# Optimization experiments

Measured on AMD Instinct MI355X. Metric: run time of the kernel, lower is better.

Reference implementation:

```python
import jax, jax.numpy as jnp
import numpy as np

N_NODES = 100_000
N_EDGES = 3_200_000
F_IN, HID, OUT = 64, 64, 6


def setup_inputs() -> dict:
    key = jax.random.key(0)
    k1, k2, k3, k4 = jax.random.split(key, 4)
    x = jax.random.normal(k1, (N_NODES, F_IN), dtype=jnp.float32)
    edge_index = jax.random.randint(k2, (2, N_EDGES), 0, N_NODES, dtype=jnp.int32)
    W1 = jax.random.normal(k3, (F_IN, HID), dtype=jnp.float32) * (1.0 / np.sqrt(F_IN))
    b1 = jnp.zeros((HID,), dtype=jnp.float32)
    W2 = jax.random.normal(k4, (HID, OUT), dtype=jnp.float32) * (1.0 / np.sqrt(HID))
    b2 = jnp.zeros((OUT,), dtype=jnp.float32)
    return {"x": x, "edge_index": edge_index, "W1": W1, "b1": b1, "W2": W2, "b2": b2}


def _gcn_conv(x, row, col, norm, W, b):
    # x: [N, F_in], row/col/norm: [E'], W: [F_in, F_out]
    n = x.shape[0]
    h = x @ W                                   # [N, F_out]
    msg = h[row] * norm[:, None]                # gather + scale, [E', F_out]
    out = jax.ops.segment_sum(msg, col, num_segments=n)  # scatter-add to targets
    return out + b


def reference(x, edge_index, W1, b1, W2, b2):
    n = x.shape[0]
    # add self-loops (PyG GCNConv default)
    loops = jnp.arange(n, dtype=edge_index.dtype)
    row = jnp.concatenate([edge_index[0], loops])  # source
    col = jnp.concatenate([edge_index[1], loops])  # target
    # symmetric normalization: deg computed at target incl. self-loops
    deg = jax.ops.segment_sum(jnp.ones_like(col, dtype=x.dtype), col, num_segments=n)
    dinv = jnp.where(deg > 0, jax.lax.rsqrt(deg), 0.0)
    norm = dinv[row] * dinv[col]                # [E']

    h = jax.nn.relu(_gcn_conv(x, row, col, norm, W1, b1))
    out = _gcn_conv(h, row, col, norm, W2, b2)
    return jnp.mean(out, axis=0)                # [OUT]
```

## Files before the change

### kernel.cpp

```cpp
#include <hip/hip_runtime.h>

#define N_NODES 100000
#define N_EDGES 3200000
#define NOUT 6

#define NPB 256
#define NBUK ((N_NODES + NPB - 1) / NPB)
#define CAP 12288
#define PCHUNK 4096
#define PNB ((N_EDGES + PCHUNK - 1) / PCHUNK)
#define SORT_CAP 10240
#define AGB (N_NODES / 32)
#define NPART (2 * AGB)

typedef __attribute__((ext_vector_type(2))) float v2f;

__global__ __launch_bounds__(512) void k_initcur(int* __restrict__ gcursor) {
    int t = threadIdx.x;
    if (t < NBUK) gcursor[t] = t * CAP;
}

__global__ __launch_bounds__(512) void k_partition(const int* __restrict__ row,
                                                   const int* __restrict__ col,
                                                   int* __restrict__ gcursor,
                                                   int* __restrict__ bedge) {
    __shared__ int hist[512];
    __shared__ int lstart[512];
    __shared__ int lcur[512];
    __shared__ int gbase[512];
    __shared__ int sscan[512];
    __shared__ int stage[PCHUNK];
    __shared__ unsigned short stageb[PCHUNK];

    const int t = threadIdx.x;
    const int c0 = blockIdx.x * PCHUNK;
    int cnt = N_EDGES - c0; if (cnt > PCHUNK) cnt = PCHUNK;

    hist[t] = 0; lcur[t] = 0;
    __syncthreads();

    int myp[8]; int myb[8];
#pragma unroll
    for (int i = 0; i < 8; ++i) {
        int p = i * 512 + t;
        myb[i] = -1;
        if (p < cnt) {
            int e = c0 + p;
            int c = col[e], r = row[e];
            int b = c >> 8;
            myp[i] = ((c & 255) << 17) | r;
            myb[i] = b;
            atomicAdd(&hist[b], 1);
        }
    }
    __syncthreads();

    int hv = hist[t];
    sscan[t] = hv;
    __syncthreads();
    for (int off = 1; off < 512; off <<= 1) {
        int u = (t >= off) ? sscan[t - off] : 0;
        __syncthreads();
        sscan[t] += u;
        __syncthreads();
    }
    lstart[t] = sscan[t] - hv;
    if (t < NBUK && hv > 0) gbase[t] = atomicAdd(&gcursor[t], hv);
    __syncthreads();

#pragma unroll
    for (int i = 0; i < 8; ++i) {
        if (myb[i] >= 0) {
            int pos = lstart[myb[i]] + atomicAdd(&lcur[myb[i]], 1);
            stage[pos] = myp[i];
            stageb[pos] = (unsigned short)myb[i];
        }
    }
    __syncthreads();

    for (int p = t; p < cnt; p += 512) {
        int b = stageb[p];
        int dst = gbase[b] + p - lstart[b];
        if (dst < (b + 1) * CAP) bedge[dst] = stage[p];
    }
}

__global__ __launch_bounds__(512) void k_bucket_sort(const int* __restrict__ gcursor,
                                                     const int* __restrict__ bedge,
                                                     float* __restrict__ dinv,
                                                     int* __restrict__ node_off,
                                                     int* __restrict__ sorted_row) {
    __shared__ int cnt[NPB];
    __shared__ int lstart[NPB];
    __shared__ int lcur[NPB];
    __shared__ int sc[NPB];
    __shared__ int stage[SORT_CAP];

    const int t = threadIdx.x;
    const int b = blockIdx.x;
    const int s = b * CAP;
    int m = gcursor[b] - s; if (m > CAP) m = CAP;
    const bool fits = (m <= SORT_CAP);

    if (t < NPB) { cnt[t] = 0; lcur[t] = 0; }
    __syncthreads();

    if (fits) {
        for (int j = t; j < m; j += 512) {
            int p = bedge[s + j];
            stage[j] = p;
            atomicAdd(&cnt[p >> 17], 1);
        }
    } else {
        for (int j = t; j < m; j += 512) atomicAdd(&cnt[bedge[s + j] >> 17], 1);
    }
    __syncthreads();

    if (t < NPB) sc[t] = cnt[t];
    __syncthreads();
    for (int off = 1; off < NPB; off <<= 1) {
        int u = 0;
        if (t < NPB && t >= off) u = sc[t - off];
        __syncthreads();
        if (t < NPB && t >= off) sc[t] += u;
        __syncthreads();
    }
    if (t < NPB) {
        int c = cnt[t];
        lstart[t] = sc[t] - c;
        node_off[b * 257 + t] = s + sc[t] - c;
        int g = b * NPB + t;
        if (g < N_NODES) dinv[g] = rsqrtf((float)c + 1.0f);
    }
    if (t == 256) node_off[b * 257 + 256] = s + m;
    __syncthreads();

    if (fits) {
        for (int j = t; j < m; j += 512) {
            int p = stage[j];
            int lc = p >> 17;
            int pos = lstart[lc] + atomicAdd(&lcur[lc], 1);
            sorted_row[s + pos] = p & 0x1FFFF;
        }
    } else {
        for (int j = t; j < m; j += 512) {
            int p = bedge[s + j];
            int lc = p >> 17;
            int pos = lstart[lc] + atomicAdd(&lcur[lc], 1);
            sorted_row[s + pos] = p & 0x1FFFF;
        }
    }
}

__global__ __launch_bounds__(256) void k_gemm1(const float* __restrict__ x,
                                               const float* __restrict__ W1,
                                               const float* __restrict__ dinv,
                                               unsigned int* __restrict__ hs1b) {
    __shared__ float Ws[64 * 64];
    __shared__ float Xs[64 * 65];
    const int tx = threadIdx.x;
    const int nodeBase = blockIdx.x * 64;

    for (int t = tx; t < 64 * 64; t += 256) Ws[t] = W1[t];

    for (int t = tx; t < 64 * 16; t += 256) {
        int r = t >> 4, c4 = t & 15;
        int g = nodeBase + r;
        float4 v = make_float4(0.f, 0.f, 0.f, 0.f);
        if (g < N_NODES) v = reinterpret_cast<const float4*>(x)[g * 16 + c4];
        float* p = &Xs[r * 65 + c4 * 4];
        p[0] = v.x; p[1] = v.y; p[2] = v.z; p[3] = v.w;
    }
    __syncthreads();

    const int nG = tx >> 4;
    const int cG = tx & 15;
    float acc[4][4] = {};
    for (int k = 0; k < 64; ++k) {
        float4 w = *reinterpret_cast<const float4*>(&Ws[k * 64 + cG * 4]);
#pragma unroll
        for (int i = 0; i < 4; ++i) {
            float xv = Xs[(nG * 4 + i) * 65 + k];
            acc[i][0] = fmaf(xv, w.x, acc[i][0]);
            acc[i][1] = fmaf(xv, w.y, acc[i][1]);
            acc[i][2] = fmaf(xv, w.z, acc[i][2]);
            acc[i][3] = fmaf(xv, w.w, acc[i][3]);
        }
    }

#pragma unroll
    for (int i = 0; i < 4; ++i) {
        int n = nodeBase + nG * 4 + i;
        if (n < N_NODES) {
            float dv = dinv[n];
            int u = __builtin_amdgcn_cvt_pk_fp8_f32(acc[i][0] * dv, acc[i][1] * dv, 0, false);
            u = __builtin_amdgcn_cvt_pk_fp8_f32(acc[i][2] * dv, acc[i][3] * dv, u, true);
            hs1b[n * 16 + cG] = (unsigned int)u;
        }
    }
}

__device__ inline void addrow8(float* __restrict__ acc, uint2 u) {
    v2f p0 = __builtin_amdgcn_cvt_pk_f32_fp8((int)u.x, false);
    v2f p1 = __builtin_amdgcn_cvt_pk_f32_fp8((int)u.x, true);
    v2f p2 = __builtin_amdgcn_cvt_pk_f32_fp8((int)u.y, false);
    v2f p3 = __builtin_amdgcn_cvt_pk_f32_fp8((int)u.y, true);
    acc[0] += p0.x; acc[1] += p0.y; acc[2] += p1.x; acc[3] += p1.y;
    acc[4] += p2.x; acc[5] += p2.y; acc[6] += p3.x; acc[7] += p3.y;
}

__global__ __launch_bounds__(256) void k_agg_l2(const int* __restrict__ node_off,
                                                const int* __restrict__ sorted_row,
                                                const unsigned int* __restrict__ hs1b,
                                                const float* __restrict__ W2,
                                                const float* __restrict__ b1,
                                                const float* __restrict__ dinv,
                                                float* __restrict__ hs2,
                                                float* __restrict__ partials) {
    __shared__ float W2s[64 * NOUT];
    __shared__ float b1s[64];
    __shared__ float pacc[8];
    const int tx = threadIdx.x;
    for (int t = tx; t < 64 * NOUT; t += 256) W2s[t] = W2[t];
    if (tx < 64) b1s[tx] = b1[tx];
    if (tx < 8) pacc[tx] = 0.f;
    __syncthreads();

    const int node = (blockIdx.x * 256 + tx) >> 3;
    const int l = tx & 7;
    const int idx = (node >> 8) * 257 + (node & 255);
    const int s = node_off[idx], e = node_off[idx + 1];
    const uint2* h8 = reinterpret_cast<const uint2*>(hs1b);

    float acc[8] = {};
    addrow8(acc, h8[node * 8 + l]);
    int j = s;
    for (; j + 4 <= e; j += 4) {
        int r0 = sorted_row[j],     r1 = sorted_row[j + 1];
        int r2 = sorted_row[j + 2], r3 = sorted_row[j + 3];
        uint2 a = h8[r0 * 8 + l];
        uint2 b = h8[r1 * 8 + l];
        uint2 c = h8[r2 * 8 + l];
        uint2 d = h8[r3 * 8 + l];
        addrow8(acc, a); addrow8(acc, b); addrow8(acc, c); addrow8(acc, d);
    }
    for (; j < e; ++j) addrow8(acc, h8[sorted_row[j] * 8 + l]);

    const float dv = dinv[node];
    float sj[NOUT] = {};
#pragma unroll
    for (int i = 0; i < 8; ++i) {
        float hv = fmaxf(fmaf(dv, acc[i], b1s[l * 8 + i]), 0.f);
#pragma unroll
        for (int q = 0; q < NOUT; ++q) sj[q] = fmaf(hv, W2s[(l * 8 + i) * NOUT + q], sj[q]);
    }
#pragma unroll
    for (int q = 0; q < NOUT; ++q) {
        sj[q] += __shfl_xor(sj[q], 1, 64);
        sj[q] += __shfl_xor(sj[q], 2, 64);
        sj[q] += __shfl_xor(sj[q], 4, 64);
    }
    if (l == 0) {
        float4 o0 = make_float4(sj[0] * dv, sj[1] * dv, sj[2] * dv, sj[3] * dv);
        float4 o1 = make_float4(sj[4] * dv, sj[5] * dv, 0.f, 0.f);
        reinterpret_cast<float4*>(hs2)[node * 2] = o0;
        reinterpret_cast<float4*>(hs2)[node * 2 + 1] = o1;
        float sc = dv * dv;
#pragma unroll
        for (int q = 0; q < NOUT; ++q) atomicAdd(&pacc[q], sj[q] * sc);
    }
    __syncthreads();
    if (tx < NOUT) partials[blockIdx.x * 8 + tx] = pacc[tx];
}

__global__ __launch_bounds__(256) void k_wsum2(const int* __restrict__ node_off,
                                               const int* __restrict__ sorted_row,
                                               const float* __restrict__ dinv,
                                               const float* __restrict__ hs2,
                                               float* __restrict__ partials) {
    const int tx = threadIdx.x;
    const int node = (blockIdx.x * 256 + tx) >> 3;
    const int l = tx & 7;
    const int idx = (node >> 8) * 257 + (node & 255);
    const int s = node_off[idx], e = node_off[idx + 1];

    float a = 0.f;
    int j = s;
    for (; j + 4 <= e; j += 4) {
        int r0 = sorted_row[j],     r1 = sorted_row[j + 1];
        int r2 = sorted_row[j + 2], r3 = sorted_row[j + 3];
        float f0 = hs2[r0 * 8 + l];
        float f1 = hs2[r1 * 8 + l];
        float f2 = hs2[r2 * 8 + l];
        float f3 = hs2[r3 * 8 + l];
        a += (f0 + f1) + (f2 + f3);
    }
    for (; j < e; ++j) a += hs2[sorted_row[j] * 8 + l];
    a *= dinv[node];

    a += __shfl_xor(a, 8, 64);
    a += __shfl_xor(a, 16, 64);
    a += __shfl_xor(a, 32, 64);
    __shared__ float wred[4][8];
    const int lane = tx & 63, w = tx >> 6;
    if (lane < 8) wred[w][lane] = a;
    __syncthreads();
    if (tx < 8)
        partials[(AGB + blockIdx.x) * 8 + tx] = wred[0][tx] + wred[1][tx] + wred[2][tx] + wred[3][tx];
}

__global__ __launch_bounds__(256) void k_reduce2(const float* __restrict__ partials,
                                                 const float* __restrict__ b2,
                                                 float* __restrict__ out) {
    __shared__ float s[256];
    for (int j = 0; j < NOUT; ++j) {
        float a = 0.f;
        for (int p = threadIdx.x; p < NPART; p += 256) a += partials[p * 8 + j];
        s[threadIdx.x] = a;
        __syncthreads();
        for (int off = 128; off > 0; off >>= 1) {
            if (threadIdx.x < off) s[threadIdx.x] += s[threadIdx.x + off];
            __syncthreads();
        }
        if (threadIdx.x == 0) out[j] = b2[j] + s[0] * (1.0f / N_NODES);
        __syncthreads();
    }
}

extern "C" void kernel_launch(void* const* d_in, const int* in_sizes, int n_in,
                              void* d_out, int out_size, void* d_ws, size_t ws_size,
                              hipStream_t stream) {
    const float* x  = (const float*)d_in[0];
    const int*   ei = (const int*)d_in[1];
    const float* W1 = (const float*)d_in[2];
    const float* b1 = (const float*)d_in[3];
    const float* W2 = (const float*)d_in[4];
    const float* b2 = (const float*)d_in[5];
    float* out = (float*)d_out;

    unsigned int* hs1b = (unsigned int*)d_ws;
    float* dinv      = (float*)(hs1b + 1600000);
    float* hs2       = dinv + 100352;
    float* partials  = hs2 + 800000;
    int*   gcursor   = (int*)(partials + 50176);
    int*   node_off  = gcursor + 512;
    int*   sorted_row= node_off + 100864;
    int*   bedge     = sorted_row + 4804608;

    const int* row = ei;
    const int* col = ei + N_EDGES;

    k_initcur<<<1, 512, 0, stream>>>(gcursor);
    k_partition<<<PNB, 512, 0, stream>>>(row, col, gcursor, bedge);
    k_bucket_sort<<<NBUK, 512, 0, stream>>>(gcursor, bedge, dinv, node_off, sorted_row);

    k_gemm1<<<(N_NODES + 63) / 64, 256, 0, stream>>>(x, W1, dinv, hs1b);

    k_agg_l2<<<AGB, 256, 0, stream>>>(node_off, sorted_row, hs1b, W2, b1, dinv, hs2, partials);

    k_wsum2<<<AGB, 256, 0, stream>>>(node_off, sorted_row, dinv, hs2, partials);

    k_reduce2<<<1, 256, 0, stream>>>(partials, b2, out);
}
```

Before: 179.8 us.

## Store layer-1 hidden features as FP4 to halve gather traffic

When the compiler provides the gfx950 scaled FP4 conversion builtins, the GEMM1 epilogue packs each node's 64 normalized hidden features as FP4 (pre-scaled by 8) instead of FP8. The layer-2 aggregation decodes them with a matching unpack, is unrolled to 8 neighbours, and undoes the scale through dinv. This halves the bytes per gathered neighbour row, but the much coarser 4-bit quantization risks accuracy. Smaller changes: edge-index loads become nontemporal, and the cursor-init kernel is replaced by a memset with bucket-relative offsets.

Result: slower. 194.7 us (+8.3%).

```diff
diff --git a/kernel.cpp b/kernel.cpp
--- a/kernel.cpp
+++ b/kernel.cpp
@@ -15,10 +15,14 @@
 
 typedef __attribute__((ext_vector_type(2))) float v2f;
 
-__global__ __launch_bounds__(512) void k_initcur(int* __restrict__ gcursor) {
-    int t = threadIdx.x;
-    if (t < NBUK) gcursor[t] = t * CAP;
-}
+#if defined(__has_builtin)
+#if __has_builtin(__builtin_amdgcn_cvt_scalef32_pk_f32_fp4) && __has_builtin(__builtin_amdgcn_cvt_scalef32_pk_fp4_f32)
+#define USE_FP4 1
+#endif
+#endif
+#ifndef USE_FP4
+#define USE_FP4 0
+#endif
 
 __global__ __launch_bounds__(512) void k_partition(const int* __restrict__ row,
                                                    const int* __restrict__ col,
@@ -80,8 +84,8 @@
 
     for (int p = t; p < cnt; p += 512) {
         int b = stageb[p];
-        int dst = gbase[b] + p - lstart[b];
-        if (dst < (b + 1) * CAP) bedge[dst] = stage[p];
+        int rel = gbase[b] + p - lstart[b];
+        if (rel < CAP) bedge[b * CAP + rel] = stage[p];
     }
 }
 
@@ -99,7 +103,7 @@
     const int t = threadIdx.x;
     const int b = blockIdx.x;
     const int s = b * CAP;
-    int m = gcursor[b] - s; if (m > CAP) m = CAP;
+    int m = gcursor[b]; if (m > CAP) m = CAP;
     const bool fits = (m <= SORT_CAP);
 
     if (t < NPB) { cnt[t] = 0; lcur[t] = 0; }
@@ -193,13 +197,30 @@
         int n = nodeBase + nG * 4 + i;
         if (n < N_NODES) {
             float dv = dinv[n];
+#if USE_FP4
+            unsigned int u = 0;
+            u = __builtin_amdgcn_cvt_scalef32_pk_fp4_f32(u, acc[i][0] * dv * 8.0f, acc[i][1] * dv * 8.0f, 1.0f, 0);
+            u = __builtin_amdgcn_cvt_scalef32_pk_fp4_f32(u, acc[i][2] * dv * 8.0f, acc[i][3] * dv * 8.0f, 1.0f, 1);
+            reinterpret_cast<unsigned short*>(hs1b)[n * 16 + cG] = (unsigned short)(u & 0xFFFFu);
+#else
             int u = __builtin_amdgcn_cvt_pk_fp8_f32(acc[i][0] * dv, acc[i][1] * dv, 0, false);
             u = __builtin_amdgcn_cvt_pk_fp8_f32(acc[i][2] * dv, acc[i][3] * dv, u, true);
             hs1b[n * 16 + cG] = (unsigned int)u;
-        }
-    }
-}
-
+#endif
+        }
+    }
+}
+
+#if USE_FP4
+__device__ inline void addrow4(float* __restrict__ acc, unsigned int u) {
+    v2f p0 = __builtin_amdgcn_cvt_scalef32_pk_f32_fp4(u, 1.0f, 0);
+    v2f p1 = __builtin_amdgcn_cvt_scalef32_pk_f32_fp4(u, 1.0f, 1);
+    v2f p2 = __builtin_amdgcn_cvt_scalef32_pk_f32_fp4(u, 1.0f, 2);
+    v2f p3 = __builtin_amdgcn_cvt_scalef32_pk_f32_fp4(u, 1.0f, 3);
+    acc[0] += p0.x; acc[1] += p0.y; acc[2] += p1.x; acc[3] += p1.y;
+    acc[4] += p2.x; acc[5] += p2.y; acc[6] += p3.x; acc[7] += p3.y;
+}
+#else
 __device__ inline void addrow8(float* __restrict__ acc, uint2 u) {
     v2f p0 = __builtin_amdgcn_cvt_pk_f32_fp8((int)u.x, false);
     v2f p1 = __builtin_amdgcn_cvt_pk_f32_fp8((int)u.x, true);
@@ -208,6 +229,7 @@
     acc[0] += p0.x; acc[1] += p0.y; acc[2] += p1.x; acc[3] += p1.y;
     acc[4] += p2.x; acc[5] += p2.y; acc[6] += p3.x; acc[7] += p3.y;
 }
+#endif
 
 __global__ __launch_bounds__(256) void k_agg_l2(const int* __restrict__ node_off,
                                                 const int* __restrict__ sorted_row,
@@ -230,27 +252,55 @@
     const int l = tx & 7;
     const int idx = (node >> 8) * 257 + (node & 255);
     const int s = node_off[idx], e = node_off[idx + 1];
+
+    float acc[8] = {};
+#if USE_FP4
+    const unsigned int* h1 = hs1b;
+    addrow4(acc, h1[node * 8 + l]);
+    int j = s;
+    for (; j + 8 <= e; j += 8) {
+        int r0 = __builtin_nontemporal_load(&sorted_row[j]);
+        int r1 = __builtin_nontemporal_load(&sorted_row[j + 1]);
+        int r2 = __builtin_nontemporal_load(&sorted_row[j + 2]);
+        int r3 = __builtin_nontemporal_load(&sorted_row[j + 3]);
+        int r4 = __builtin_nontemporal_load(&sorted_row[j + 4]);
+        int r5 = __builtin_nontemporal_load(&sorted_row[j + 5]);
+        int r6 = __builtin_nontemporal_load(&sorted_row[j + 6]);
+        int r7 = __builtin_nontemporal_load(&sorted_row[j + 7]);
+        unsigned int g0 = h1[r0 * 8 + l], g1 = h1[r1 * 8 + l];
+        unsigned int g2 = h1[r2 * 8 + l], g3 = h1[r3 * 8 + l];
+        unsigned int g4 = h1[r4 * 8 + l], g5 = h1[r5 * 8 + l];
+        unsigned int g6 = h1[r6 * 8 + l], g7 = h1[r7 * 8 + l];
+        addrow4(acc, g0); addrow4(acc, g1); addrow4(acc, g2); addrow4(acc, g3);
+        addrow4(acc, g4); addrow4(acc, g5); addrow4(acc, g6); addrow4(acc, g7);
+    }
+    for (; j < e; ++j) addrow4(acc, h1[__builtin_nontemporal_load(&sorted_row[j]) * 8 + l]);
+    const float dv = dinv[node];
+    const float dva = dv * 0.125f;
+#else
     const uint2* h8 = reinterpret_cast<const uint2*>(hs1b);
-
-    float acc[8] = {};
     addrow8(acc, h8[node * 8 + l]);
     int j = s;
     for (; j + 4 <= e; j += 4) {
-        int r0 = sorted_row[j],     r1 = sorted_row[j + 1];
-        int r2 = sorted_row[j + 2], r3 = sorted_row[j + 3];
+        int r0 = __builtin_nontemporal_load(&sorted_row[j]);
+        int r1 = __builtin_nontemporal_load(&sorted_row[j + 1]);
+        int r2 = __builtin_nontemporal_load(&sorted_row[j + 2]);
+        int r3 = __builtin_nontemporal_load(&sorted_row[j + 3]);
         uint2 a = h8[r0 * 8 + l];
         uint2 b = h8[r1 * 8 + l];
         uint2 c = h8[r2 * 8 + l];
         uint2 d = h8[r3 * 8 + l];
         addrow8(acc, a); addrow8(acc, b); addrow8(acc, c); addrow8(acc, d);
     }
-    for (; j < e; ++j) addrow8(acc, h8[sorted_row[j] * 8 + l]);
-
+    for (; j < e; ++j) addrow8(acc, h8[__builtin_nontemporal_load(&sorted_row[j]) * 8 + l]);
     const float dv = dinv[node];
+    const float dva = dv;
+#endif
+
     float sj[NOUT] = {};
 #pragma unroll
     for (int i = 0; i < 8; ++i) {
-        float hv = fmaxf(fmaf(dv, acc[i], b1s[l * 8 + i]), 0.f);
+        float hv = fmaxf(fmaf(dva, acc[i], b1s[l * 8 + i]), 0.f);
 #pragma unroll
         for (int q = 0; q < NOUT; ++q) sj[q] = fmaf(hv, W2s[(l * 8 + i) * NOUT + q], sj[q]);
     }
@@ -287,15 +337,17 @@
     float a = 0.f;
     int j = s;
     for (; j + 4 <= e; j += 4) {
-        int r0 = sorted_row[j],     r1 = sorted_row[j + 1];
-        int r2 = sorted_row[j + 2], r3 = sorted_row[j + 3];
+        int r0 = __builtin_nontemporal_load(&sorted_row[j]);
+        int r1 = __builtin_nontemporal_load(&sorted_row[j + 1]);
+        int r2 = __builtin_nontemporal_load(&sorted_row[j + 2]);
+        int r3 = __builtin_nontemporal_load(&sorted_row[j + 3]);
         float f0 = hs2[r0 * 8 + l];
         float f1 = hs2[r1 * 8 + l];
         float f2 = hs2[r2 * 8 + l];
         float f3 = hs2[r3 * 8 + l];
         a += (f0 + f1) + (f2 + f3);
     }
-    for (; j < e; ++j) a += hs2[sorted_row[j] * 8 + l];
+    for (; j < e; ++j) a += hs2[__builtin_nontemporal_load(&sorted_row[j]) * 8 + l];
     a *= dinv[node];
 
     a += __shfl_xor(a, 8, 64);
@@ -350,7 +402,7 @@
     const int* row = ei;
     const int* col = ei + N_EDGES;
 
-    k_initcur<<<1, 512, 0, stream>>>(gcursor);
+    hipMemsetAsync(gcursor, 0, NBUK * sizeof(int), stream);
     k_partition<<<PNB, 512, 0, stream>>>(row, col, gcursor, bedge);
     k_bucket_sort<<<NBUK, 512, 0, stream>>>(gcursor, bedge, dinv, node_off, sorted_row);
 
```

## Split per-node edge aggregation across two lane groups, add fp16 packed accumulation

Applied to the files above, without the earlier changes.

Each destination node's edge range is now split in half and handled by two 8-lane groups in both k_agg_l2 and k_wsum2, with the halves combined by a lane shuffle. This doubles the grid so more memory loads are in flight during the latency-bound gather. When the packed fp8-to-fp16 conversion builtin is available, the layer-1 gather accumulates in packed half precision, which saves conversion and add instructions but risks lost precision or overflow. The init-cursor kernel is replaced by a memset with bucket-relative cursors, and the partials buffer is enlarged to fit the larger grid.

New measurement: 210.7 us. +17.2%, slower.

```diff
diff --git a/kernel.cpp b/kernel.cpp
--- a/kernel.cpp
+++ b/kernel.cpp
@@ -10,15 +10,23 @@
 #define PCHUNK 4096
 #define PNB ((N_EDGES + PCHUNK - 1) / PCHUNK)
 #define SORT_CAP 10240
-#define AGB (N_NODES / 32)
+#define AGB (N_NODES * 2 / 32)
 #define NPART (2 * AGB)
 
 typedef __attribute__((ext_vector_type(2))) float v2f;
 
-__global__ __launch_bounds__(512) void k_initcur(int* __restrict__ gcursor) {
-    int t = threadIdx.x;
-    if (t < NBUK) gcursor[t] = t * CAP;
-}
+#if defined(__has_builtin)
+#if __has_builtin(__builtin_amdgcn_cvt_scalef32_pk_f16_fp8)
+#define USE_PKH 1
+#endif
+#endif
+#ifndef USE_PKH
+#define USE_PKH 0
+#endif
+
+#if USE_PKH
+typedef _Float16 v2h __attribute__((ext_vector_type(2)));
+#endif
 
 __global__ __launch_bounds__(512) void k_partition(const int* __restrict__ row,
                                                    const int* __restrict__ col,
@@ -80,8 +88,8 @@
 
     for (int p = t; p < cnt; p += 512) {
         int b = stageb[p];
-        int dst = gbase[b] + p - lstart[b];
-        if (dst < (b + 1) * CAP) bedge[dst] = stage[p];
+        int rel = gbase[b] + p - lstart[b];
+        if (rel < CAP) bedge[b * CAP + rel] = stage[p];
     }
 }
 
@@ -99,7 +107,7 @@
     const int t = threadIdx.x;
     const int b = blockIdx.x;
     const int s = b * CAP;
-    int m = gcursor[b] - s; if (m > CAP) m = CAP;
+    int m = gcursor[b]; if (m > CAP) m = CAP;
     const bool fits = (m <= SORT_CAP);
 
     if (t < NPB) { cnt[t] = 0; lcur[t] = 0; }
@@ -208,6 +216,15 @@
     acc[0] += p0.x; acc[1] += p0.y; acc[2] += p1.x; acc[3] += p1.y;
     acc[4] += p2.x; acc[5] += p2.y; acc[6] += p3.x; acc[7] += p3.y;
 }
+
+#if USE_PKH
+__device__ inline void addrowh(v2h* __restrict__ acch, uint2 u) {
+    acch[0] += __builtin_amdgcn_cvt_scalef32_pk_f16_fp8((int)u.x, 1.0f, false);
+    acch[1] += __builtin_amdgcn_cvt_scalef32_pk_f16_fp8((int)u.x, 1.0f, true);
+    acch[2] += __builtin_amdgcn_cvt_scalef32_pk_f16_fp8((int)u.y, 1.0f, false);
+    acch[3] += __builtin_amdgcn_cvt_scalef32_pk_f16_fp8((int)u.y, 1.0f, true);
+}
+#endif
 
 __global__ __launch_bounds__(256) void k_agg_l2(const int* __restrict__ node_off,
                                                 const int* __restrict__ sorted_row,
@@ -226,31 +243,59 @@
     if (tx < 8) pacc[tx] = 0.f;
     __syncthreads();
 
-    const int node = (blockIdx.x * 256 + tx) >> 3;
+    const int unit = (blockIdx.x * 256 + tx) >> 3;
+    const int node = unit >> 1;
+    const int half = unit & 1;
     const int l = tx & 7;
     const int idx = (node >> 8) * 257 + (node & 255);
-    const int s = node_off[idx], e = node_off[idx + 1];
-    const uint2* h8 = reinterpret_cast<const uint2*>(hs1b);
-
-    float acc[8] = {};
-    addrow8(acc, h8[node * 8 + l]);
+    const int s0 = node_off[idx], e0 = node_off[idx + 1];
+    const int hl = (e0 - s0) >> 1;
+    const int s = half ? (s0 + hl) : s0;
+    const int e = half ? e0 : (s0 + hl);
+    const uint2* hsrc = reinterpret_cast<const uint2*>(hs1b);
+
+    float accf[8];
+#if USE_PKH
+    v2h acch[4] = {};
+    if (half == 0) addrowh(acch, hsrc[node * 8 + l]);
     int j = s;
     for (; j + 4 <= e; j += 4) {
         int r0 = sorted_row[j],     r1 = sorted_row[j + 1];
         int r2 = sorted_row[j + 2], r3 = sorted_row[j + 3];
-        uint2 a = h8[r0 * 8 + l];
-        uint2 b = h8[r1 * 8 + l];
-        uint2 c = h8[r2 * 8 + l];
-        uint2 d = h8[r3 * 8 + l];
-        addrow8(acc, a); addrow8(acc, b); addrow8(acc, c); addrow8(acc, d);
-    }
-    for (; j < e; ++j) addrow8(acc, h8[sorted_row[j] * 8 + l]);
+        uint2 a = hsrc[r0 * 8 + l];
+        uint2 b = hsrc[r1 * 8 + l];
+        uint2 c = hsrc[r2 * 8 + l];
+        uint2 d = hsrc[r3 * 8 + l];
+        addrowh(acch, a); addrowh(acch, b); addrowh(acch, c); addrowh(acch, d);
+    }
+    for (; j < e; ++j) addrowh(acch, hsrc[sorted_row[j] * 8 + l]);
+#pragma unroll
+    for (int i = 0; i < 4; ++i) { accf[2 * i] = (float)acch[i].x; accf[2 * i + 1] = (float)acch[i].y; }
+#else
+#pragma unroll
+    for (int i = 0; i < 8; ++i) accf[i] = 0.f;
+    if (half == 0) addrow8(accf, hsrc[node * 8 + l]);
+    int j = s;
+    for (; j + 4 <= e; j += 4) {
+        int r0 = sorted_row[j],     r1 = sorted_row[j + 1];
+        int r2 = sorted_row[j + 2], r3 = sorted_row[j + 3];
+        uint2 a = hsrc[r0 * 8 + l];
+        uint2 b = hsrc[r1 * 8 + l];
+        uint2 c = hsrc[r2 * 8 + l];
+        uint2 d = hsrc[r3 * 8 + l];
+        addrow8(accf, a); addrow8(accf, b); addrow8(accf, c); addrow8(accf, d);
+    }
+    for (; j < e; ++j) addrow8(accf, hsrc[sorted_row[j] * 8 + l]);
+#endif
+
+#pragma unroll
+    for (int i = 0; i < 8; ++i) accf[i] += __shfl_xor(accf[i], 8, 64);
 
     const float dv = dinv[node];
     float sj[NOUT] = {};
 #pragma unroll
     for (int i = 0; i < 8; ++i) {
-        float hv = fmaxf(fmaf(dv, acc[i], b1s[l * 8 + i]), 0.f);
+        float hv = fmaxf(fmaf(dv, accf[i], b1s[l * 8 + i]), 0.f);
 #pragma unroll
         for (int q = 0; q < NOUT; ++q) sj[q] = fmaf(hv, W2s[(l * 8 + i) * NOUT + q], sj[q]);
     }
@@ -260,7 +305,7 @@
         sj[q] += __shfl_xor(sj[q], 2, 64);
         sj[q] += __shfl_xor(sj[q], 4, 64);
     }
-    if (l == 0) {
+    if (l == 0 && half == 0) {
         float4 o0 = make_float4(sj[0] * dv, sj[1] * dv, sj[2] * dv, sj[3] * dv);
         float4 o1 = make_float4(sj[4] * dv, sj[5] * dv, 0.f, 0.f);
         reinterpret_cast<float4*>(hs2)[node * 2] = o0;
@@ -279,10 +324,15 @@
                                                const float* __restrict__ hs2,
                                                float* __restrict__ partials) {
     const int tx = threadIdx.x;
-    const int node = (blockIdx.x * 256 + tx) >> 3;
+    const int unit = (blockIdx.x * 256 + tx) >> 3;
+    const int node = unit >> 1;
+    const int half = unit & 1;
     const int l = tx & 7;
     const int idx = (node >> 8) * 257 + (node & 255);
-    const int s = node_off[idx], e = node_off[idx + 1];
+    const int s0 = node_off[idx], e0 = node_off[idx + 1];
+    const int hl = (e0 - s0) >> 1;
+    const int s = half ? (s0 + hl) : s0;
+    const int e = half ? e0 : (s0 + hl);
 
     float a = 0.f;
     int j = s;
@@ -342,7 +392,7 @@
     float* dinv      = (float*)(hs1b + 1600000);
     float* hs2       = dinv + 100352;
     float* partials  = hs2 + 800000;
-    int*   gcursor   = (int*)(partials + 50176);
+    int*   gcursor   = (int*)(partials + 100352);
     int*   node_off  = gcursor + 512;
     int*   sorted_row= node_off + 100864;
     int*   bedge     = sorted_row + 4804608;
@@ -350,7 +400,7 @@
     const int* row = ei;
     const int* col = ei + N_EDGES;
 
-    k_initcur<<<1, 512, 0, stream>>>(gcursor);
+    hipMemsetAsync(gcursor, 0, NBUK * sizeof(int), stream);
     k_partition<<<PNB, 512, 0, stream>>>(row, col, gcursor, bedge);
     k_bucket_sort<<<NBUK, 512, 0, stream>>>(gcursor, bedge, dinv, node_off, sorted_row);
 
```
